# Kernel tuning notes

Hardware: AMD Instinct MI355X
Metric: run time of the kernel (lower is better)

Reference implementation:

```python
import jax, jax.numpy as jnp
import numpy as np

# ---- static configuration (mirrors init_kwargs) ----
B, NCAM = 1, 6
FC, FH, FW = 128, 16, 44              # featureShape
ORFH, ORFW = 128, 352                 # transformedImgShape H, W
D_ST, D_END, D_STEP = 1.0, 49.0, 1.0
D = int(np.arange(D_ST, D_END, D_STEP).shape[0])   # 48 depth bins
OUTC = 128
XB = (-50.0, 50.0, 1.0)
YB = (-50.0, 50.0, 1.0)
BEV_H = int((YB[1] - YB[0]) / YB[2])  # 100
BEV_W = int((XB[1] - XB[0]) / XB[2])  # 100
THRESH = 0.05                         # opacity_filter
ERR_TOL = 1.0                         # error_tolerance
COV_DILATE = 0.3                      # 3DGS low-pass on 2D cov diagonal
ALPHA_MAX = 0.99
ALPHA_MIN = 1.0 / 255.0
BN_EPS = 1e-3


def _frustum():
    ds = jnp.arange(D_ST, D_END, D_STEP, dtype=jnp.float32)[:, None, None]
    xs = jnp.linspace(0.0, ORFW - 1.0, FW, dtype=jnp.float32)[None, None, :]
    ys = jnp.linspace(0.0, ORFH - 1.0, FH, dtype=jnp.float32)[None, :, None]
    shp = (D, FH, FW)
    return jnp.stack([jnp.broadcast_to(xs, shp), jnp.broadcast_to(ys, shp),
                      jnp.broadcast_to(ds, shp)], axis=-1)  # [D,FH,FW,3]


def _conv(x, w, b, pad):
    y = jax.lax.conv_general_dilated(x, w, (1, 1), [(pad, pad), (pad, pad)],
                                     dimension_numbers=('NCHW', 'OIHW', 'NCHW'))
    return y + b[None, :, None, None]


def _bn(x, g, beta, m, v):
    # eval-mode BatchNorm2d with running stats
    inv = g / jnp.sqrt(v + BN_EPS)
    return (x - m[None, :, None, None]) * inv[None, :, None, None] + beta[None, :, None, None]


def _rasterize(features, means, cov6, opac):
    """Differentiable BEV Gaussian splatting (alpha compositing in index order).
    features [G,C], means [G,3] (normalized to [-1,1]), cov6 [G,6]=(xx,xy,xz,yy,yz,zz), opac [G].
    """
    h, w = BEV_H, BEV_W
    sh, sw = h / 2.0, w / 2.0                 # h/FoVy, w/FoVx with FoV=2
    op = jnp.where(opac > THRESH, opac, 0.0)  # opacity cull (variable-length mask in torch)
    # full_proj_transform: row0 -> row index (y), row1 -> col index (x)
    py = h / 2.0 - sh * means[:, 1]
    px = w / 2.0 - sw * means[:, 0]
    # 2D covariance in (py,px) basis: J Sigma3 J^T with J = [[0,-sh,0],[-sw,0,0]]
    a = sh * sh * cov6[:, 3] + COV_DILATE     # var along py (from Sigma_yy)
    b = sh * sw * cov6[:, 1]                  # cov(py,px) (from Sigma_xy)
    c = sw * sw * cov6[:, 0] + COV_DILATE     # var along px (from Sigma_xx)
    det = a * c - b * b
    op = jnp.where(det > 0.0, op, 0.0)
    inv_det = 1.0 / jnp.where(det > 0.0, det, 1.0)
    ys = jnp.arange(h, dtype=jnp.float32)
    xs = jnp.arange(w, dtype=jnp.float32)
    dy = py[None, :] - ys[:, None]            # [h,G]
    dx = px[None, :] - xs[:, None]            # [w,G]
    # power = -0.5 d^T Sigma2^{-1} d, Sigma2^{-1} = [[c,-b],[-b,a]]/det
    power = (-0.5 * (c * inv_det) * dy * dy)[:, None, :] \
            + (-0.5 * (a * inv_det) * dx * dx)[None, :, :] \
            + (b * inv_det) * dy[:, None, :] * dx[None, :, :]   # [h,w,G]
    alpha = jnp.minimum(ALPHA_MAX, op * jnp.exp(jnp.minimum(power, 0.0)))
    alpha = jnp.where(alpha < ALPHA_MIN, 0.0, alpha)
    T = jnp.cumprod(1.0 - alpha, axis=-1)
    T_excl = jnp.concatenate([jnp.ones_like(T[..., :1]), T[..., :-1]], axis=-1)
    wgt = alpha * T_excl                      # [h,w,G]
    bev = jnp.einsum('hwg,gc->chw', wgt, features)   # bg color = 0
    return bev


def reference(cam2ego_rot, cam2ego_trans, cam_intrins, post_cam2ego_rot, post_cam2ego_trans,
              img_feats, conv1_w, conv1_b, bn1_g, bn1_b, bn1_m, bn1_v,
              conv2_w, conv2_b, bn2_g, bn2_b, bn2_m, bn2_v, conv3_w, conv3_b):
    # --- geometry lifting ---
    frustum = _frustum()                                             # [D,FH,FW,3]
    pts = frustum[None, None] - post_cam2ego_trans[:, :, None, None, None, :]
    pts = jnp.einsum('bnij,bndhwj->bndhwi', jnp.linalg.inv(post_cam2ego_rot), pts)
    pts = jnp.concatenate([pts[..., :2] * pts[..., 2:3], pts[..., 2:3]], axis=-1)
    combine = cam2ego_rot @ jnp.linalg.inv(cam_intrins)
    geometry = jnp.einsum('bnij,bndhwj->bndhwi', combine, pts) \
               + cam2ego_trans[:, :, None, None, None, :]            # [B,N,D,FH,FW,3]
    # --- depth net ---
    x = img_feats.reshape(B * NCAM, FC, FH, FW)
    x = jax.nn.relu(_bn(_conv(x, conv1_w, conv1_b, 1), bn1_g, bn1_b, bn1_m, bn1_v))
    x = jax.nn.relu(_bn(_conv(x, conv2_w, conv2_b, 1), bn2_g, bn2_b, bn2_m, bn2_v))
    x = _conv(x, conv3_w, conv3_b, 0)                                # [B*N, OUTC+D+1, H, W]
    depth_prob = jax.nn.softmax(x[:, :D], axis=1).reshape(B, NCAM, D, FH, FW)
    opac = jax.nn.sigmoid(x[:, D:D + 1]).reshape(B, NCAM, FH, FW)
    feats = x[:, D + 1:].reshape(B, NCAM, OUTC, FH, FW)
    # --- per-pixel Gaussian moments over the depth distribution ---
    means3d = jnp.einsum('bndhw,bndhwi->bnhwi', depth_prob, geometry)
    delta = means3d[:, :, None] - geometry                           # [B,N,D,FH,FW,3]
    cov = jnp.einsum('bndhw,bndhwi,bndhwj->bnhwij', depth_prob, delta, delta)
    cov = cov * (ERR_TOL ** 2 / 9.0)
    # --- normalize to BEV frame ---
    center = jnp.array([(XB[0] + XB[1]) / 2.0, (YB[0] + YB[1]) / 2.0, 0.0], jnp.float32)
    scale = jnp.array([2.0 / (XB[1] - XB[0]), 2.0 / (YB[1] - YB[0]), 1.0], jnp.float32)
    means_n = (means3d - center) * scale
    cov_n = cov * (scale[:, None] * scale[None, :])
    cov6 = jnp.stack([cov_n[..., 0, 0], cov_n[..., 0, 1], cov_n[..., 0, 2],
                      cov_n[..., 1, 1], cov_n[..., 1, 2], cov_n[..., 2, 2]], axis=-1)
    G = NCAM * FH * FW
    f = jnp.transpose(feats, (0, 1, 3, 4, 2)).reshape(B, G, OUTC)
    m = means_n.reshape(B, G, 3)
    c6 = cov6.reshape(B, G, 6)
    o = opac.reshape(B, G)
    bev = jax.vmap(_rasterize)(f, m, c6, o)                          # [B,OUTC,BEV_H,BEV_W]
    return bev


def setup_inputs() -> dict:
    key = jax.random.key(0)
    ks = jax.random.split(key, 16)
    eye = jnp.eye(3, dtype=jnp.float32)
    cam2ego_rot = eye + 0.05 * jax.random.normal(ks[0], (B, NCAM, 3, 3), jnp.float32)
    cam2ego_trans = 0.5 * jax.random.normal(ks[1], (B, NCAM, 3), jnp.float32)
    intr = jnp.array([[260.0, 0.0, ORFW / 2.0], [0.0, 260.0, ORFH / 2.0], [0.0, 0.0, 1.0]], jnp.float32)
    cam_intrins = jnp.broadcast_to(intr, (B, NCAM, 3, 3)) * (1.0 + 0.01 * jax.random.normal(ks[2], (B, NCAM, 1, 1), jnp.float32))
    post_cam2ego_rot = eye + 0.01 * jax.random.normal(ks[3], (B, NCAM, 3, 3), jnp.float32)
    post_cam2ego_trans = 2.0 * jax.random.normal(ks[4], (B, NCAM, 3), jnp.float32)
    img_feats = jax.random.normal(ks[5], (B, NCAM, FC, FH, FW), jnp.float32)
    def cw(k, o, i, kh, kw):
        return jax.random.normal(k, (o, i, kh, kw), jnp.float32) / np.sqrt(i * kh * kw)
    inp = dict(cam2ego_rot=cam2ego_rot, cam2ego_trans=cam2ego_trans, cam_intrins=cam_intrins,
               post_cam2ego_rot=post_cam2ego_rot, post_cam2ego_trans=post_cam2ego_trans,
               img_feats=img_feats,
               conv1_w=cw(ks[6], FC, FC, 3, 3), conv1_b=jnp.zeros((FC,), jnp.float32),
               bn1_g=jnp.ones((FC,), jnp.float32), bn1_b=0.1 * jax.random.normal(ks[7], (FC,), jnp.float32),
               bn1_m=jnp.zeros((FC,), jnp.float32), bn1_v=jnp.ones((FC,), jnp.float32),
               conv2_w=cw(ks[8], FC, FC, 3, 3), conv2_b=jnp.zeros((FC,), jnp.float32),
               bn2_g=jnp.ones((FC,), jnp.float32), bn2_b=0.1 * jax.random.normal(ks[9], (FC,), jnp.float32),
               bn2_m=jnp.zeros((FC,), jnp.float32), bn2_v=jnp.ones((FC,), jnp.float32),
               conv3_w=cw(ks[10], OUTC + D + 1, FC, 1, 1),
               conv3_b=jnp.zeros((OUTC + D + 1,), jnp.float32))
    return inp
```

## Files before the change

kernel.cpp:

```cpp
#include <hip/hip_runtime.h>
#include <math.h>

#define NCAM 6
#define FHh 16
#define FWw 44
#define PIX 704
#define FCc 128
#define DB 48
#define C3 177
#define C3PAD 192
#define KCONV 1152
#define NG 4224
#define BEVN 10000
#define NSPLIT 3
#define SG 1408
#define TH_LOG (-5.5412635f)

#define OFF_WT1    0
#define OFF_WT2    147456
#define OFF_WT3    294912
#define OFF_GEO    319488
#define OFF_X1     724992
#define OFF_X2     1265664
#define OFF_X3     1806336
#define OFF_PART   2553984
#define OFF_PRM    4716672
#define OFF_PRM2   4733568
#define OFF_FEATT  4742016
#define OFF_SF     0
#define OFF_SP     3840000

typedef __attribute__((ext_vector_type(8))) short bf16x8;
typedef __attribute__((ext_vector_type(4))) float f32x4;
typedef __attribute__((ext_vector_type(4))) int i32x4;

__device__ __forceinline__ unsigned short f2bf(float x) {
  unsigned u = __float_as_uint(x);
  return (unsigned short)((u + 0x7FFF + ((u >> 16) & 1)) >> 16);
}
__device__ __forceinline__ float bf2f(unsigned short h) {
  return __uint_as_float(((unsigned)h) << 16);
}

__device__ __forceinline__ void inv3(const float* A, float* I) {
  float a=A[0],b=A[1],c=A[2],d=A[3],e=A[4],f=A[5],g=A[6],h=A[7],i=A[8];
  float c0 = e*i - f*h, c1 = f*g - d*i, c2 = d*h - e*g;
  float det = a*c0 + b*c1 + c*c2;
  float id = 1.f/det;
  I[0]=c0*id; I[1]=(c*h-b*i)*id; I[2]=(b*f-c*e)*id;
  I[3]=c1*id; I[4]=(a*i-c*g)*id; I[5]=(c*d-a*f)*id;
  I[6]=c2*id; I[7]=(b*g-a*h)*id; I[8]=(a*e-b*d)*id;
}

__global__ void k_geom(const float* __restrict__ rot, const float* __restrict__ intr,
                       const float* __restrict__ post_rot,
                       const float* __restrict__ trans, const float* __restrict__ post_trans,
                       float* __restrict__ ws) {
  __shared__ float sm[NCAM][24];
  if (threadIdx.x < NCAM) {
    int n = threadIdx.x;
    float ip[9], ii[9];
    inv3(post_rot + n*9, ip);
    inv3(intr + n*9, ii);
    const float* R = rot + n*9;
    for (int j = 0; j < 9; ++j) sm[n][j] = ip[j];
    for (int r = 0; r < 3; ++r)
      for (int c = 0; c < 3; ++c) {
        float s = 0.f;
        for (int k = 0; k < 3; ++k) s += R[r*3+k]*ii[k*3+c];
        sm[n][9 + r*3 + c] = s;
      }
  }
  __syncthreads();
  int idx = blockIdx.x*256 + threadIdx.x;
  if (idx >= NCAM*DB*PIX) return;
  int n = idx / (DB*PIX);
  int rem = idx % (DB*PIX);
  int d = rem / PIX;
  int hw = rem % PIX;
  int h = hw / FWw, w = hw % FWw;
  float fx = w * (351.0f/43.0f);
  float fy = h * (127.0f/15.0f);
  float fz = 1.0f + (float)d;
  const float* pt = post_trans + n*3;
  float v0 = fx - pt[0], v1 = fy - pt[1], v2 = fz - pt[2];
  const float* m = sm[n];
  float x = m[0]*v0 + m[1]*v1 + m[2]*v2;
  float y = m[3]*v0 + m[4]*v1 + m[5]*v2;
  float z = m[6]*v0 + m[7]*v1 + m[8]*v2;
  float q0 = x*z, q1 = y*z, q2 = z;
  const float* c = m + 9;
  const float* t = trans + n*3;
  float gx = c[0]*q0 + c[1]*q1 + c[2]*q2 + t[0];
  float gy = c[3]*q0 + c[4]*q1 + c[5]*q2 + t[1];
  ((float2*)(ws + OFF_GEO))[idx] = make_float2(gx, gy);
}

__global__ void k_wtrans(const float* __restrict__ w1, const float* __restrict__ w2,
                         const float* __restrict__ w3, float* __restrict__ ws) {
  int e = blockIdx.x*256 + threadIdx.x;
  if (e < 147456) {
    float v1 = w1[e], v2 = w2[e];
    unsigned short h1 = f2bf(v1), h2 = f2bf(v2);
    unsigned short l1 = f2bf(v1 - bf2f(h1)), l2 = f2bf(v2 - bf2f(h2));
    unsigned short* wt1 = (unsigned short*)(ws + OFF_WT1);
    unsigned short* wt2 = (unsigned short*)(ws + OFF_WT2);
    wt1[e] = h1; wt1[147456 + e] = l1;
    wt2[e] = h2; wt2[147456 + e] = l2;
  }
  if (e < 192*128) {
    int oc = e >> 7, k = e & 127;
    float v = (oc < C3) ? w3[oc*FCc + k] : 0.f;
    unsigned short h = f2bf(v);
    unsigned short* wt3 = (unsigned short*)(ws + OFF_WT3);
    wt3[e] = h; wt3[24576 + e] = f2bf(v - bf2f(h));
  }
}

#define LROW 20

__global__ __launch_bounds__(256) void k_gemm_mfma(
    const float* __restrict__ in, const float* ws, float* __restrict__ part, int woff)
{
  __shared__ int alds[2][64*LROW];
  __shared__ int blds[2][64*LROW];
  int tid = threadIdx.x;
  int px0 = blockIdx.x * 64;
  int oc0 = blockIdx.y * 64;
  int z = blockIdx.z; int n = z >> 2, ks = z & 3;
  const unsigned short* whi = (const unsigned short*)(ws + woff);
  const unsigned short* wlo = whi + 147456;
  const float* inn = in + (size_t)n*FCc*PIX;
  int wv = tid >> 6, lane = tid & 63;
  int a_oc = tid >> 2, a_kq = tid & 3;
  int b_px = tid & 63, b_kq = tid >> 6;
  int p = px0 + b_px; int b_y = p / FWw, b_x = p - b_y*FWw;
  int k00 = ks * 288;

  i32x4 pa_h, pa_l; float bv[8];
  auto issueA = [&](int s) {
    size_t gi = (size_t)(oc0 + a_oc)*KCONV + (k00 + s*32 + a_kq*8);
    pa_h = *(const i32x4*)(whi + gi);
    pa_l = *(const i32x4*)(wlo + gi);
  };
  auto issueB = [&](int s) {
    #pragma unroll
    for (int j = 0; j < 8; ++j) {
      int k = k00 + s*32 + b_kq*8 + j;
      int ic = k / 9, tap = k - ic*9;
      int ky = tap / 3, kx = tap - ky*3;
      int yy = b_y + ky - 1, xx = b_x + kx - 1;
      float v = 0.f;
      if ((unsigned)yy < FHh && (unsigned)xx < FWw) v = inn[(size_t)ic*PIX + yy*FWw + xx];
      bv[j] = v;
    }
  };

  f32x4 a00 = {0.f,0.f,0.f,0.f}, a01 = a00, a10 = a00, a11 = a00;
  int ocr = (wv >> 1) * 32, pxr = (wv & 1) * 32;
  int dq = (lane >> 4) * 4;
  int rA0 = (ocr + (lane & 15)) * LROW + dq;
  int rA1 = rA0 + 16*LROW;
  int rB0 = (pxr + (lane & 15)) * LROW + dq;
  int rB1 = rB0 + 16*LROW;
  int aw = a_oc*LROW + a_kq*4;
  int bw = b_px*LROW + b_kq*4;

  issueA(0); issueB(0);
  for (int s = 0; s < 9; ++s) {
    __syncthreads();
    *(i32x4*)&alds[0][aw] = pa_h;
    *(i32x4*)&alds[1][aw] = pa_l;
    {
      i32x4 vh, vl;
      int th[8], tl[8];
      #pragma unroll
      for (int j = 0; j < 8; ++j) {
        unsigned short h = f2bf(bv[j]);
        th[j] = h; tl[j] = f2bf(bv[j] - bf2f(h));
      }
      vh.x = th[0]|(th[1]<<16); vh.y = th[2]|(th[3]<<16);
      vh.z = th[4]|(th[5]<<16); vh.w = th[6]|(th[7]<<16);
      vl.x = tl[0]|(tl[1]<<16); vl.y = tl[2]|(tl[3]<<16);
      vl.z = tl[4]|(tl[5]<<16); vl.w = tl[6]|(tl[7]<<16);
      *(i32x4*)&blds[0][bw] = vh;
      *(i32x4*)&blds[1][bw] = vl;
    }
    __syncthreads();
    if (s < 8) { issueA(s+1); issueB(s+1); }
    bf16x8 ah0 = *(bf16x8*)&alds[0][rA0], ah1 = *(bf16x8*)&alds[0][rA1];
    bf16x8 al0 = *(bf16x8*)&alds[1][rA0], al1 = *(bf16x8*)&alds[1][rA1];
    bf16x8 bh0 = *(bf16x8*)&blds[0][rB0], bh1 = *(bf16x8*)&blds[0][rB1];
    bf16x8 bl0 = *(bf16x8*)&blds[1][rB0], bl1 = *(bf16x8*)&blds[1][rB1];
    a00 = __builtin_amdgcn_mfma_f32_16x16x32_bf16(ah0, bh0, a00, 0, 0, 0);
    a01 = __builtin_amdgcn_mfma_f32_16x16x32_bf16(ah0, bh1, a01, 0, 0, 0);
    a10 = __builtin_amdgcn_mfma_f32_16x16x32_bf16(ah1, bh0, a10, 0, 0, 0);
    a11 = __builtin_amdgcn_mfma_f32_16x16x32_bf16(ah1, bh1, a11, 0, 0, 0);
    a00 = __builtin_amdgcn_mfma_f32_16x16x32_bf16(ah0, bl0, a00, 0, 0, 0);
    a01 = __builtin_amdgcn_mfma_f32_16x16x32_bf16(ah0, bl1, a01, 0, 0, 0);
    a10 = __builtin_amdgcn_mfma_f32_16x16x32_bf16(ah1, bl0, a10, 0, 0, 0);
    a11 = __builtin_amdgcn_mfma_f32_16x16x32_bf16(ah1, bl1, a11, 0, 0, 0);
    a00 = __builtin_amdgcn_mfma_f32_16x16x32_bf16(al0, bh0, a00, 0, 0, 0);
    a01 = __builtin_amdgcn_mfma_f32_16x16x32_bf16(al0, bh1, a01, 0, 0, 0);
    a10 = __builtin_amdgcn_mfma_f32_16x16x32_bf16(al1, bh0, a10, 0, 0, 0);
    a11 = __builtin_amdgcn_mfma_f32_16x16x32_bf16(al1, bh1, a11, 0, 0, 0);
  }
  float* pp = part + (size_t)(ks*NCAM + n)*FCc*PIX;
  int ocb = oc0 + ocr + ((lane >> 4) << 2);
  int pxb = px0 + pxr + (lane & 15);
  #pragma unroll
  for (int i = 0; i < 4; ++i) {
    pp[(size_t)(ocb + i)*PIX + pxb]           = a00[i];
    pp[(size_t)(ocb + i)*PIX + pxb + 16]      = a01[i];
    pp[(size_t)(ocb + 16 + i)*PIX + pxb]      = a10[i];
    pp[(size_t)(ocb + 16 + i)*PIX + pxb + 16] = a11[i];
  }
}

__global__ __launch_bounds__(256) void k_gemm_mfma3(
    const float* __restrict__ in, const float* ws,
    const float* __restrict__ bias, float* __restrict__ outbuf)
{
  __shared__ int alds[2][64*LROW];
  __shared__ int blds[2][64*LROW];
  int tid = threadIdx.x;
  int px0 = blockIdx.x * 64;
  int oc0 = blockIdx.y * 64;
  int n = blockIdx.z;
  const unsigned short* whi = (const unsigned short*)(ws + OFF_WT3);
  const unsigned short* wlo = whi + 24576;
  const float* inn = in + (size_t)n*FCc*PIX;
  int wv = tid >> 6, lane = tid & 63;
  int a_oc = tid >> 2, a_kq = tid & 3;
  int b_px = tid & 63, b_kq = tid >> 6;
  int p = px0 + b_px;

  i32x4 pa_h, pa_l; float bvv[8];
  auto issueA = [&](int s) {
    size_t gi = (size_t)(oc0 + a_oc)*128 + (s*32 + a_kq*8);
    pa_h = *(const i32x4*)(whi + gi);
    pa_l = *(const i32x4*)(wlo + gi);
  };
  auto issueB = [&](int s) {
    #pragma unroll
    for (int j = 0; j < 8; ++j) {
      int ic = s*32 + b_kq*8 + j;
      bvv[j] = inn[(size_t)ic*PIX + p];
    }
  };

  f32x4 a00 = {0.f,0.f,0.f,0.f}, a01 = a00, a10 = a00, a11 = a00;
  int ocr = (wv >> 1) * 32, pxr = (wv & 1) * 32;
  int dq = (lane >> 4) * 4;
  int rA0 = (ocr + (lane & 15)) * LROW + dq;
  int rA1 = rA0 + 16*LROW;
  int rB0 = (pxr + (lane & 15)) * LROW + dq;
  int rB1 = rB0 + 16*LROW;
  int aw = a_oc*LROW + a_kq*4;
  int bw = b_px*LROW + b_kq*4;

  issueA(0); issueB(0);
  for (int s = 0; s < 4; ++s) {
    __syncthreads();
    *(i32x4*)&alds[0][aw] = pa_h;
    *(i32x4*)&alds[1][aw] = pa_l;
    {
      i32x4 vh, vl;
      int th[8], tl[8];
      #pragma unroll
      for (int j = 0; j < 8; ++j) {
        unsigned short h = f2bf(bvv[j]);
        th[j] = h; tl[j] = f2bf(bvv[j] - bf2f(h));
      }
      vh.x = th[0]|(th[1]<<16); vh.y = th[2]|(th[3]<<16);
      vh.z = th[4]|(th[5]<<16); vh.w = th[6]|(th[7]<<16);
      vl.x = tl[0]|(tl[1]<<16); vl.y = tl[2]|(tl[3]<<16);
      vl.z = tl[4]|(tl[5]<<16); vl.w = tl[6]|(tl[7]<<16);
      *(i32x4*)&blds[0][bw] = vh;
      *(i32x4*)&blds[1][bw] = vl;
    }
    __syncthreads();
    if (s < 3) { issueA(s+1); issueB(s+1); }
    bf16x8 ah0 = *(bf16x8*)&alds[0][rA0], ah1 = *(bf16x8*)&alds[0][rA1];
    bf16x8 al0 = *(bf16x8*)&alds[1][rA0], al1 = *(bf16x8*)&alds[1][rA1];
    bf16x8 bh0 = *(bf16x8*)&blds[0][rB0], bh1 = *(bf16x8*)&blds[0][rB1];
    bf16x8 bl0 = *(bf16x8*)&blds[1][rB0], bl1 = *(bf16x8*)&blds[1][rB1];
    a00 = __builtin_amdgcn_mfma_f32_16x16x32_bf16(ah0, bh0, a00, 0, 0, 0);
    a01 = __builtin_amdgcn_mfma_f32_16x16x32_bf16(ah0, bh1, a01, 0, 0, 0);
    a10 = __builtin_amdgcn_mfma_f32_16x16x32_bf16(ah1, bh0, a10, 0, 0, 0);
    a11 = __builtin_amdgcn_mfma_f32_16x16x32_bf16(ah1, bh1, a11, 0, 0, 0);
    a00 = __builtin_amdgcn_mfma_f32_16x16x32_bf16(ah0, bl0, a00, 0, 0, 0);
    a01 = __builtin_amdgcn_mfma_f32_16x16x32_bf16(ah0, bl1, a01, 0, 0, 0);
    a10 = __builtin_amdgcn_mfma_f32_16x16x32_bf16(ah1, bl0, a10, 0, 0, 0);
    a11 = __builtin_amdgcn_mfma_f32_16x16x32_bf16(ah1, bl1, a11, 0, 0, 0);
    a00 = __builtin_amdgcn_mfma_f32_16x16x32_bf16(al0, bh0, a00, 0, 0, 0);
    a01 = __builtin_amdgcn_mfma_f32_16x16x32_bf16(al0, bh1, a01, 0, 0, 0);
    a10 = __builtin_amdgcn_mfma_f32_16x16x32_bf16(al1, bh0, a10, 0, 0, 0);
    a11 = __builtin_amdgcn_mfma_f32_16x16x32_bf16(al1, bh1, a11, 0, 0, 0);
  }
  int ocb = oc0 + ocr + ((lane >> 4) << 2);
  int pxb = px0 + pxr + (lane & 15);
  #pragma unroll
  for (int i = 0; i < 4; ++i) {
    int o0 = ocb + i, o1 = ocb + 16 + i;
    if (o0 < C3) {
      float b = bias[o0];
      outbuf[(size_t)(n*C3 + o0)*PIX + pxb]      = a00[i] + b;
      outbuf[(size_t)(n*C3 + o0)*PIX + pxb + 16] = a01[i] + b;
    }
    if (o1 < C3) {
      float b = bias[o1];
      outbuf[(size_t)(n*C3 + o1)*PIX + pxb]      = a10[i] + b;
      outbuf[(size_t)(n*C3 + o1)*PIX + pxb + 16] = a11[i] + b;
    }
  }
}

__global__ void k_epi_bn(const float* __restrict__ part, const float* __restrict__ cb,
                         const float* __restrict__ g, const float* __restrict__ be,
                         const float* __restrict__ mn, const float* __restrict__ vr,
                         float* __restrict__ out, int KSPLIT)
{
  int idx = blockIdx.x*256 + threadIdx.x;
  if (idx >= NCAM*FCc*176) return;
  int px4 = idx % 176;
  int t = idx / 176;
  int oc = t % FCc;
  int n = t / FCc;
  float4 s = {0.f,0.f,0.f,0.f};
  for (int ks = 0; ks < KSPLIT; ++ks) {
    const float4* p = (const float4*)(part + (size_t)((ks*NCAM+n)*FCc + oc)*PIX);
    float4 v = p[px4];
    s.x += v.x; s.y += v.y; s.z += v.z; s.w += v.w;
  }
  float inv = g[oc] * rsqrtf(vr[oc] + 1e-3f);
  float sh = (cb[oc] - mn[oc]) * inv + be[oc];
  float4 o;
  o.x = fmaxf(s.x*inv + sh, 0.f);
  o.y = fmaxf(s.y*inv + sh, 0.f);
  o.z = fmaxf(s.z*inv + sh, 0.f);
  o.w = fmaxf(s.w*inv + sh, 0.f);
  ((float4*)(out + (size_t)(n*FCc + oc)*PIX))[px4] = o;
}

__global__ void k_moments(float* __restrict__ ws) {
  int wid  = (blockIdx.x * 256 + threadIdx.x) >> 6;
  int lane = threadIdx.x & 63;
  int n = wid / PIX, hw = wid % PIX;
  const float* x3 = ws + OFF_X3 + (size_t)n*C3*PIX + hw;
  float logit = (lane < DB) ? x3[(size_t)lane*PIX] : -1e30f;
  float mx = logit;
  for (int off = 1; off < 64; off <<= 1) mx = fmaxf(mx, __shfl_xor(mx, off));
  float e = (lane < DB) ? expf(logit - mx) : 0.f;
  float s = e;
  for (int off = 1; off < 64; off <<= 1) s += __shfl_xor(s, off);
  float p = e / s;
  float gx = 0.f, gy = 0.f;
  if (lane < DB) {
    float2 g2 = ((const float2*)(ws + OFF_GEO))[(size_t)(n*DB + lane)*PIX + hw];
    gx = g2.x; gy = g2.y;
  }
  float sx = p*gx;
  for (int off = 1; off < 64; off <<= 1) sx += __shfl_xor(sx, off);
  float sy = p*gy;
  for (int off = 1; off < 64; off <<= 1) sy += __shfl_xor(sy, off);
  float dx = gx - sx, dy = gy - sy;
  float c00 = p*dx*dx, c01 = p*dx*dy, c11 = p*dy*dy;
  for (int off = 1; off < 64; off <<= 1) c00 += __shfl_xor(c00, off);
  for (int off = 1; off < 64; off <<= 1) c01 += __shfl_xor(c01, off);
  for (int off = 1; off < 64; off <<= 1) c11 += __shfl_xor(c11, off);
  float opl = x3[(size_t)DB*PIX];
  float opac = 1.f / (1.f + expf(-opl));
  float a = c11*(1.f/9.f) + 0.3f;
  float b = c01*(1.f/9.f);
  float c = c00*(1.f/9.f) + 0.3f;
  float py = 50.f - sy;
  float px = 50.f - sx;
  float det = a*c - b*b;
  float op = (opac > 0.05f) ? opac : 0.f;
  float invd = 1.f;
  if (det > 0.f) invd = 1.f/det; else op = 0.f;
  if (lane == 0) {
    float lop = (op > 0.f) ? logf(op) : -1e30f;
    ((float4*)(ws + OFF_PRM))[wid]  = make_float4(py, px, -0.5f*c*invd, -0.5f*a*invd);
    ((float2*)(ws + OFF_PRM2))[wid] = make_float2(b*invd, lop);
  }
  float* ft = ws + OFF_FEATT + (size_t)wid*128;
  ft[lane]      = x3[(size_t)(DB + 1 + lane)*PIX];
  ft[lane + 64] = x3[(size_t)(DB + 1 + lane + 64)*PIX];
}

template<int CTRL, int RMASK>
__device__ __forceinline__ float dpp_mul(float v) {
  int t = __builtin_amdgcn_update_dpp(0x3f800000, __float_as_int(v), CTRL, RMASK, 0xF, false);
  return v * __int_as_float(t);
}

__global__ __launch_bounds__(512) void k_raster(const float* __restrict__ ws,
                                                float* __restrict__ wsout) {
  __shared__ float4 s4[SG];
  __shared__ float2 s2[SG];
  int lane = threadIdx.x & 63, wv = threadIdx.x >> 6;
  int split = blockIdx.x / 1250;
  int pxb   = blockIdx.x % 1250;
  int pix = pxb * 8 + wv;
  float yi = (float)(pix / 100), xi = (float)(pix % 100);
  int gbase = split * SG;
  const float4* prm4 = (const float4*)(ws + OFF_PRM) + gbase;
  const float2* prm2 = (const float2*)(ws + OFF_PRM2) + gbase;
  const float2* ft = (const float2*)(ws + OFF_FEATT);
  for (int i = threadIdx.x; i < SG; i += 512) {
    s4[i] = prm4[i];
    s2[i] = prm2[i];
  }
  __syncthreads();
  float T = 1.f, ax = 0.f, ay = 0.f;
  for (int gl = 0; gl < SG; gl += 64) {
    float4 c4 = s4[gl + lane];
    float2 c2 = s2[gl + lane];
    float dyv = c4.x - yi, dxv = c4.y - xi;
    float pw = c4.z*dyv*dyv + c4.w*dxv*dxv + c2.x*dyv*dxv;
    float t  = pw + c2.y;
    bool hit = (t >= TH_LOG);
    unsigned long long m0 = __ballot(hit);
    if (m0) {
      float alpha = __expf(fminf(t, c2.y));
      alpha = fminf(alpha, 0.99f);
      alpha = hit ? alpha : 0.f;
      float P = 1.f - alpha;
      P = dpp_mul<0x111, 0xF>(P);
      P = dpp_mul<0x112, 0xF>(P);
      P = dpp_mul<0x114, 0xF>(P);
      P = dpp_mul<0x118, 0xF>(P);
      P = dpp_mul<0x142, 0xA>(P);
      P = dpp_mul<0x143, 0xC>(P);
      float E = __int_as_float(__builtin_amdgcn_update_dpp(
                  0x3f800000, __float_as_int(P), 0x138, 0xF, 0xF, false));
      float w = alpha * T * E;
      T *= __int_as_float(__builtin_amdgcn_readlane(__float_as_int(P), 63));
      unsigned long long mask = __ballot(w > 1e-9f);
      int g0 = gbase + gl;
      while (mask) {
        int jj[8];
        #pragma unroll
        for (int b = 0; b < 8; ++b) {
          if (mask) { jj[b] = __builtin_ctzll(mask); mask &= mask - 1ull; }
          else jj[b] = -1;
        }
        float2 fb[8]; float wb[8];
        #pragma unroll
        for (int b = 0; b < 8; ++b) {
          int j = (jj[b] >= 0) ? jj[b] : jj[0];
          fb[b] = ft[(size_t)(g0 + j)*64 + lane];
          wb[b] = (jj[b] >= 0)
            ? __int_as_float(__builtin_amdgcn_readlane(__float_as_int(w), jj[b]))
            : 0.f;
        }
        #pragma unroll
        for (int b = 0; b < 8; ++b) { ax += wb[b]*fb[b].x; ay += wb[b]*fb[b].y; }
      }
      if (T < 1e-7f) break;
    }
  }
  float* sf = wsout + OFF_SF + ((size_t)split*BEVN + pix)*128;
  sf[2*lane]   = ax;
  sf[2*lane+1] = ay;
  if (lane == 0) (wsout + OFF_SP)[split*BEVN + pix] = T;
}

__global__ __launch_bounds__(512) void k_combine(const float* __restrict__ ws,
                                                 float* __restrict__ out) {
  int lane = threadIdx.x & 63, wv = threadIdx.x >> 6;
  int pix = blockIdx.x * 8 + wv;
  const float* sp = ws + OFF_SP;
  float P0 = sp[pix], P1 = sp[BEVN + pix];
  const float2* f0 = (const float2*)(ws + OFF_SF + (size_t)pix*128);
  const float2* f1 = (const float2*)(ws + OFF_SF + ((size_t)BEVN + pix)*128);
  const float2* f2 = (const float2*)(ws + OFF_SF + ((size_t)2*BEVN + pix)*128);
  float2 a = f0[lane], b = f1[lane], c = f2[lane];
  float w1 = P0, w2 = P0*P1;
  float ox = a.x + w1*b.x + w2*c.x;
  float oy = a.y + w1*b.y + w2*c.y;
  out[(size_t)(2*lane)*BEVN + pix]   = ox;
  out[(size_t)(2*lane+1)*BEVN + pix] = oy;
}

extern "C" void kernel_launch(void* const* d_in, const int* in_sizes, int n_in,
                              void* d_out, int out_size, void* d_ws, size_t ws_size,
                              hipStream_t stream) {
  const float* rot        = (const float*)d_in[0];
  const float* trans      = (const float*)d_in[1];
  const float* intr       = (const float*)d_in[2];
  const float* post_rot   = (const float*)d_in[3];
  const float* post_trans = (const float*)d_in[4];
  const float* img        = (const float*)d_in[5];
  const float* w1  = (const float*)d_in[6];
  const float* b1  = (const float*)d_in[7];
  const float* g1  = (const float*)d_in[8];
  const float* be1 = (const float*)d_in[9];
  const float* m1  = (const float*)d_in[10];
  const float* v1  = (const float*)d_in[11];
  const float* w2  = (const float*)d_in[12];
  const float* b2  = (const float*)d_in[13];
  const float* g2  = (const float*)d_in[14];
  const float* be2 = (const float*)d_in[15];
  const float* m2  = (const float*)d_in[16];
  const float* v2  = (const float*)d_in[17];
  const float* w3  = (const float*)d_in[18];
  const float* b3  = (const float*)d_in[19];
  float* ws  = (float*)d_ws;
  float* out = (float*)d_out;

  k_wtrans<<<576, 256, 0, stream>>>(w1, w2, w3, ws);
  k_geom<<<792, 256, 0, stream>>>(rot, intr, post_rot, trans, post_trans, ws);

  k_gemm_mfma<<<dim3(11,2,24), 256, 0, stream>>>(img, ws, ws+OFF_PART, OFF_WT1);
  k_epi_bn<<<528, 256, 0, stream>>>(ws+OFF_PART, b1, g1, be1, m1, v1, ws+OFF_X1, 4);
  k_gemm_mfma<<<dim3(11,2,24), 256, 0, stream>>>(ws+OFF_X1, ws, ws+OFF_PART, OFF_WT2);
  k_epi_bn<<<528, 256, 0, stream>>>(ws+OFF_PART, b2, g2, be2, m2, v2, ws+OFF_X2, 4);
  k_gemm_mfma3<<<dim3(11,3,6), 256, 0, stream>>>(ws+OFF_X2, ws, b3, ws+OFF_X3);

  k_moments<<<1056, 256, 0, stream>>>(ws);
  k_raster<<<3750, 512, 0, stream>>>(ws, ws);
  k_combine<<<1250, 512, 0, stream>>>(ws, out);
}
```

Before: 123.4 us.

## Drop split-K conv GEMM, fuse BN-ReLU epilogue, merge prep kernels

The two 3x3 conv GEMMs no longer split K four ways into partial buffers followed by a separate BN+ReLU reduction kernel. Each block now computes a 32x32 output tile over the full K=1152 in 36 steps and applies bias, BatchNorm and ReLU directly in its epilogue. The weight-transform and geometry kernels are merged into one launch. This removes two kernel launches per conv plus the partial-sum round trip through memory. In exchange each block runs a much longer serial K loop with one small MFMA tile per wave, which gives less reuse per LDS load.

```diff
diff --git a/kernel.cpp b/kernel.cpp
--- a/kernel.cpp
+++ b/kernel.cpp
@@ -8,7 +8,6 @@
 #define FCc 128
 #define DB 48
 #define C3 177
-#define C3PAD 192
 #define KCONV 1152
 #define NG 4224
 #define BEVN 10000
@@ -23,7 +22,6 @@
 #define OFF_X1     724992
 #define OFF_X2     1265664
 #define OFF_X3     1806336
-#define OFF_PART   2553984
 #define OFF_PRM    4716672
 #define OFF_PRM2   4733568
 #define OFF_FEATT  4742016
@@ -33,6 +31,7 @@
 typedef __attribute__((ext_vector_type(8))) short bf16x8;
 typedef __attribute__((ext_vector_type(4))) float f32x4;
 typedef __attribute__((ext_vector_type(4))) int i32x4;
+typedef __attribute__((ext_vector_type(2))) int i32x2;
 
 __device__ __forceinline__ unsigned short f2bf(float x) {
   unsigned u = __float_as_uint(x);
@@ -52,101 +51,103 @@
   I[6]=c2*id; I[7]=(b*g-a*h)*id; I[8]=(a*e-b*d)*id;
 }
 
-__global__ void k_geom(const float* __restrict__ rot, const float* __restrict__ intr,
+__global__ void k_prep(const float* __restrict__ rot, const float* __restrict__ intr,
                        const float* __restrict__ post_rot,
                        const float* __restrict__ trans, const float* __restrict__ post_trans,
-                       float* __restrict__ ws) {
-  __shared__ float sm[NCAM][24];
-  if (threadIdx.x < NCAM) {
-    int n = threadIdx.x;
-    float ip[9], ii[9];
-    inv3(post_rot + n*9, ip);
-    inv3(intr + n*9, ii);
-    const float* R = rot + n*9;
-    for (int j = 0; j < 9; ++j) sm[n][j] = ip[j];
-    for (int r = 0; r < 3; ++r)
-      for (int c = 0; c < 3; ++c) {
-        float s = 0.f;
-        for (int k = 0; k < 3; ++k) s += R[r*3+k]*ii[k*3+c];
-        sm[n][9 + r*3 + c] = s;
-      }
-  }
-  __syncthreads();
-  int idx = blockIdx.x*256 + threadIdx.x;
-  if (idx >= NCAM*DB*PIX) return;
-  int n = idx / (DB*PIX);
-  int rem = idx % (DB*PIX);
-  int d = rem / PIX;
-  int hw = rem % PIX;
-  int h = hw / FWw, w = hw % FWw;
-  float fx = w * (351.0f/43.0f);
-  float fy = h * (127.0f/15.0f);
-  float fz = 1.0f + (float)d;
-  const float* pt = post_trans + n*3;
-  float v0 = fx - pt[0], v1 = fy - pt[1], v2 = fz - pt[2];
-  const float* m = sm[n];
-  float x = m[0]*v0 + m[1]*v1 + m[2]*v2;
-  float y = m[3]*v0 + m[4]*v1 + m[5]*v2;
-  float z = m[6]*v0 + m[7]*v1 + m[8]*v2;
-  float q0 = x*z, q1 = y*z, q2 = z;
-  const float* c = m + 9;
-  const float* t = trans + n*3;
-  float gx = c[0]*q0 + c[1]*q1 + c[2]*q2 + t[0];
-  float gy = c[3]*q0 + c[4]*q1 + c[5]*q2 + t[1];
-  ((float2*)(ws + OFF_GEO))[idx] = make_float2(gx, gy);
-}
-
-__global__ void k_wtrans(const float* __restrict__ w1, const float* __restrict__ w2,
-                         const float* __restrict__ w3, float* __restrict__ ws) {
-  int e = blockIdx.x*256 + threadIdx.x;
-  if (e < 147456) {
-    float v1 = w1[e], v2 = w2[e];
-    unsigned short h1 = f2bf(v1), h2 = f2bf(v2);
-    unsigned short l1 = f2bf(v1 - bf2f(h1)), l2 = f2bf(v2 - bf2f(h2));
-    unsigned short* wt1 = (unsigned short*)(ws + OFF_WT1);
-    unsigned short* wt2 = (unsigned short*)(ws + OFF_WT2);
-    wt1[e] = h1; wt1[147456 + e] = l1;
-    wt2[e] = h2; wt2[147456 + e] = l2;
-  }
-  if (e < 192*128) {
-    int oc = e >> 7, k = e & 127;
-    float v = (oc < C3) ? w3[oc*FCc + k] : 0.f;
-    unsigned short h = f2bf(v);
-    unsigned short* wt3 = (unsigned short*)(ws + OFF_WT3);
-    wt3[e] = h; wt3[24576 + e] = f2bf(v - bf2f(h));
+                       const float* __restrict__ w1, const float* __restrict__ w2,
+                       const float* __restrict__ w3, float* __restrict__ ws) {
+  if (blockIdx.x < 792) {
+    __shared__ float sm[NCAM][24];
+    if (threadIdx.x < NCAM) {
+      int n = threadIdx.x;
+      float ip[9], ii[9];
+      inv3(post_rot + n*9, ip);
+      inv3(intr + n*9, ii);
+      const float* R = rot + n*9;
+      for (int j = 0; j < 9; ++j) sm[n][j] = ip[j];
+      for (int r = 0; r < 3; ++r)
+        for (int c = 0; c < 3; ++c) {
+          float s = 0.f;
+          for (int k = 0; k < 3; ++k) s += R[r*3+k]*ii[k*3+c];
+          sm[n][9 + r*3 + c] = s;
+        }
+    }
+    __syncthreads();
+    int idx = blockIdx.x*256 + threadIdx.x;
+    if (idx >= NCAM*DB*PIX) return;
+    int n = idx / (DB*PIX);
+    int rem = idx % (DB*PIX);
+    int d = rem / PIX;
+    int hw = rem % PIX;
+    int h = hw / FWw, w = hw % FWw;
+    float fx = w * (351.0f/43.0f);
+    float fy = h * (127.0f/15.0f);
+    float fz = 1.0f + (float)d;
+    const float* pt = post_trans + n*3;
+    float v0 = fx - pt[0], v1 = fy - pt[1], v2 = fz - pt[2];
+    const float* m = sm[n];
+    float x = m[0]*v0 + m[1]*v1 + m[2]*v2;
+    float y = m[3]*v0 + m[4]*v1 + m[5]*v2;
+    float z = m[6]*v0 + m[7]*v1 + m[8]*v2;
+    float q0 = x*z, q1 = y*z, q2 = z;
+    const float* c = m + 9;
+    const float* t = trans + n*3;
+    float gx = c[0]*q0 + c[1]*q1 + c[2]*q2 + t[0];
+    float gy = c[3]*q0 + c[4]*q1 + c[5]*q2 + t[1];
+    ((float2*)(ws + OFF_GEO))[idx] = make_float2(gx, gy);
+  } else {
+    int e = (blockIdx.x - 792)*256 + threadIdx.x;
+    if (e < 147456) {
+      float v1 = w1[e], v2 = w2[e];
+      unsigned short h1 = f2bf(v1), h2 = f2bf(v2);
+      unsigned short l1 = f2bf(v1 - bf2f(h1)), l2 = f2bf(v2 - bf2f(h2));
+      unsigned short* wt1 = (unsigned short*)(ws + OFF_WT1);
+      unsigned short* wt2 = (unsigned short*)(ws + OFF_WT2);
+      wt1[e] = h1; wt1[147456 + e] = l1;
+      wt2[e] = h2; wt2[147456 + e] = l2;
+    }
+    if (e < 192*128) {
+      int oc = e >> 7, k = e & 127;
+      float v = (oc < C3) ? w3[oc*FCc + k] : 0.f;
+      unsigned short h = f2bf(v);
+      unsigned short* wt3 = (unsigned short*)(ws + OFF_WT3);
+      wt3[e] = h; wt3[24576 + e] = f2bf(v - bf2f(h));
+    }
   }
 }
 
 #define LROW 20
 
-__global__ __launch_bounds__(256) void k_gemm_mfma(
-    const float* __restrict__ in, const float* ws, float* __restrict__ part, int woff)
+__global__ __launch_bounds__(256) void k_gemm_mfma32(
+    const float* __restrict__ in, const float* ws, int woff,
+    const float* __restrict__ cb, const float* __restrict__ g,
+    const float* __restrict__ be, const float* __restrict__ mn,
+    const float* __restrict__ vr, float* __restrict__ outbuf)
 {
-  __shared__ int alds[2][64*LROW];
-  __shared__ int blds[2][64*LROW];
+  __shared__ int alds[2][32*LROW];
+  __shared__ int blds[2][32*LROW];
   int tid = threadIdx.x;
-  int px0 = blockIdx.x * 64;
-  int oc0 = blockIdx.y * 64;
-  int z = blockIdx.z; int n = z >> 2, ks = z & 3;
+  int px0 = blockIdx.x * 32;
+  int oc0 = blockIdx.y * 32;
+  int n = blockIdx.z;
   const unsigned short* whi = (const unsigned short*)(ws + woff);
   const unsigned short* wlo = whi + 147456;
   const float* inn = in + (size_t)n*FCc*PIX;
   int wv = tid >> 6, lane = tid & 63;
-  int a_oc = tid >> 2, a_kq = tid & 3;
-  int b_px = tid & 63, b_kq = tid >> 6;
+  int a_oc = tid >> 3, a_kq = tid & 7;
+  int b_px = tid & 31, b_kq = tid >> 5;
   int p = px0 + b_px; int b_y = p / FWw, b_x = p - b_y*FWw;
-  int k00 = ks * 288;
-
-  i32x4 pa_h, pa_l; float bv[8];
+
+  i32x2 pa_h, pa_l; float bv[4];
   auto issueA = [&](int s) {
-    size_t gi = (size_t)(oc0 + a_oc)*KCONV + (k00 + s*32 + a_kq*8);
-    pa_h = *(const i32x4*)(whi + gi);
-    pa_l = *(const i32x4*)(wlo + gi);
+    size_t gi = (size_t)(oc0 + a_oc)*KCONV + (s*32 + a_kq*4);
+    pa_h = *(const i32x2*)(whi + gi);
+    pa_l = *(const i32x2*)(wlo + gi);
   };
   auto issueB = [&](int s) {
     #pragma unroll
-    for (int j = 0; j < 8; ++j) {
-      int k = k00 + s*32 + b_kq*8 + j;
+    for (int j = 0; j < 4; ++j) {
+      int k = s*32 + b_kq*4 + j;
       int ic = k / 9, tap = k - ic*9;
       int ky = tap / 3, kx = tap - ky*3;
       int yy = b_y + ky - 1, xx = b_x + kx - 1;
@@ -156,64 +157,50 @@
     }
   };
 
-  f32x4 a00 = {0.f,0.f,0.f,0.f}, a01 = a00, a10 = a00, a11 = a00;
-  int ocr = (wv >> 1) * 32, pxr = (wv & 1) * 32;
+  f32x4 acc = {0.f,0.f,0.f,0.f};
+  int ocr = (wv >> 1) * 16, pxr = (wv & 1) * 16;
   int dq = (lane >> 4) * 4;
-  int rA0 = (ocr + (lane & 15)) * LROW + dq;
-  int rA1 = rA0 + 16*LROW;
-  int rB0 = (pxr + (lane & 15)) * LROW + dq;
-  int rB1 = rB0 + 16*LROW;
-  int aw = a_oc*LROW + a_kq*4;
-  int bw = b_px*LROW + b_kq*4;
+  int rA = (ocr + (lane & 15)) * LROW + dq;
+  int rB = (pxr + (lane & 15)) * LROW + dq;
+  int aw = a_oc*LROW + a_kq*2;
+  int bw = b_px*LROW + b_kq*2;
 
   issueA(0); issueB(0);
-  for (int s = 0; s < 9; ++s) {
+  for (int s = 0; s < 36; ++s) {
     __syncthreads();
-    *(i32x4*)&alds[0][aw] = pa_h;
-    *(i32x4*)&alds[1][aw] = pa_l;
+    *(i32x2*)&alds[0][aw] = pa_h;
+    *(i32x2*)&alds[1][aw] = pa_l;
     {
-      i32x4 vh, vl;
-      int th[8], tl[8];
+      i32x2 vh, vl;
+      int th[4], tl[4];
       #pragma unroll
-      for (int j = 0; j < 8; ++j) {
+      for (int j = 0; j < 4; ++j) {
         unsigned short h = f2bf(bv[j]);
         th[j] = h; tl[j] = f2bf(bv[j] - bf2f(h));
       }
       vh.x = th[0]|(th[1]<<16); vh.y = th[2]|(th[3]<<16);
-      vh.z = th[4]|(th[5]<<16); vh.w = th[6]|(th[7]<<16);
       vl.x = tl[0]|(tl[1]<<16); vl.y = tl[2]|(tl[3]<<16);
-      vl.z = tl[4]|(tl[5]<<16); vl.w = tl[6]|(tl[7]<<16);
-      *(i32x4*)&blds[0][bw] = vh;
-      *(i32x4*)&blds[1][bw] = vl;
+      *(i32x2*)&blds[0][bw] = vh;
+      *(i32x2*)&blds[1][bw] = vl;
     }
     __syncthreads();
-    if (s < 8) { issueA(s+1); issueB(s+1); }
-    bf16x8 ah0 = *(bf16x8*)&alds[0][rA0], ah1 = *(bf16x8*)&alds[0][rA1];
-    bf16x8 al0 = *(bf16x8*)&alds[1][rA0], al1 = *(bf16x8*)&alds[1][rA1];
-    bf16x8 bh0 = *(bf16x8*)&blds[0][rB0], bh1 = *(bf16x8*)&blds[0][rB1];
-    bf16x8 bl0 = *(bf16x8*)&blds[1][rB0], bl1 = *(bf16x8*)&blds[1][rB1];
-    a00 = __builtin_amdgcn_mfma_f32_16x16x32_bf16(ah0, bh0, a00, 0, 0, 0);
-    a01 = __builtin_amdgcn_mfma_f32_16x16x32_bf16(ah0, bh1, a01, 0, 0, 0);
-    a10 = __builtin_amdgcn_mfma_f32_16x16x32_bf16(ah1, bh0, a10, 0, 0, 0);
-    a11 = __builtin_amdgcn_mfma_f32_16x16x32_bf16(ah1, bh1, a11, 0, 0, 0);
-    a00 = __builtin_amdgcn_mfma_f32_16x16x32_bf16(ah0, bl0, a00, 0, 0, 0);
-    a01 = __builtin_amdgcn_mfma_f32_16x16x32_bf16(ah0, bl1, a01, 0, 0, 0);
-    a10 = __builtin_amdgcn_mfma_f32_16x16x32_bf16(ah1, bl0, a10, 0, 0, 0);
-    a11 = __builtin_amdgcn_mfma_f32_16x16x32_bf16(ah1, bl1, a11, 0, 0, 0);
-    a00 = __builtin_amdgcn_mfma_f32_16x16x32_bf16(al0, bh0, a00, 0, 0, 0);
-    a01 = __builtin_amdgcn_mfma_f32_16x16x32_bf16(al0, bh1, a01, 0, 0, 0);
-    a10 = __builtin_amdgcn_mfma_f32_16x16x32_bf16(al1, bh0, a10, 0, 0, 0);
-    a11 = __builtin_amdgcn_mfma_f32_16x16x32_bf16(al1, bh1, a11, 0, 0, 0);
-  }
-  float* pp = part + (size_t)(ks*NCAM + n)*FCc*PIX;
+    if (s < 35) { issueA(s+1); issueB(s+1); }
+    bf16x8 ah = *(bf16x8*)&alds[0][rA];
+    bf16x8 al = *(bf16x8*)&alds[1][rA];
+    bf16x8 bh = *(bf16x8*)&blds[0][rB];
+    bf16x8 bl = *(bf16x8*)&blds[1][rB];
+    acc = __builtin_amdgcn_mfma_f32_16x16x32_bf16(ah, bh, acc, 0, 0, 0);
+    acc = __builtin_amdgcn_mfma_f32_16x16x32_bf16(ah, bl, acc, 0, 0, 0);
+    acc = __builtin_amdgcn_mfma_f32_16x16x32_bf16(al, bh, acc, 0, 0, 0);
+  }
   int ocb = oc0 + ocr + ((lane >> 4) << 2);
   int pxb = px0 + pxr + (lane & 15);
   #pragma unroll
   for (int i = 0; i < 4; ++i) {
-    pp[(size_t)(ocb + i)*PIX + pxb]           = a00[i];
-    pp[(size_t)(ocb + i)*PIX + pxb + 16]      = a01[i];
-    pp[(size_t)(ocb + 16 + i)*PIX + pxb]      = a10[i];
-    pp[(size_t)(ocb + 16 + i)*PIX + pxb + 16] = a11[i];
+    int oc = ocb + i;
+    float inv = g[oc] * rsqrtf(vr[oc] + 1e-3f);
+    float sh = (cb[oc] - mn[oc]) * inv + be[oc];
+    outbuf[(size_t)(n*FCc + oc)*PIX + pxb] = fmaxf(acc[i]*inv + sh, 0.f);
   }
 }
 
@@ -314,33 +301,6 @@
       outbuf[(size_t)(n*C3 + o1)*PIX + pxb + 16] = a11[i] + b;
     }
   }
-}
-
-__global__ void k_epi_bn(const float* __restrict__ part, const float* __restrict__ cb,
-                         const float* __restrict__ g, const float* __restrict__ be,
-                         const float* __restrict__ mn, const float* __restrict__ vr,
-                         float* __restrict__ out, int KSPLIT)
-{
-  int idx = blockIdx.x*256 + threadIdx.x;
-  if (idx >= NCAM*FCc*176) return;
-  int px4 = idx % 176;
-  int t = idx / 176;
-  int oc = t % FCc;
-  int n = t / FCc;
-  float4 s = {0.f,0.f,0.f,0.f};
-  for (int ks = 0; ks < KSPLIT; ++ks) {
-    const float4* p = (const float4*)(part + (size_t)((ks*NCAM+n)*FCc + oc)*PIX);
-    float4 v = p[px4];
-    s.x += v.x; s.y += v.y; s.z += v.z; s.w += v.w;
-  }
-  float inv = g[oc] * rsqrtf(vr[oc] + 1e-3f);
-  float sh = (cb[oc] - mn[oc]) * inv + be[oc];
-  float4 o;
-  o.x = fmaxf(s.x*inv + sh, 0.f);
-  o.y = fmaxf(s.y*inv + sh, 0.f);
-  o.z = fmaxf(s.z*inv + sh, 0.f);
-  o.w = fmaxf(s.w*inv + sh, 0.f);
-  ((float4*)(out + (size_t)(n*FCc + oc)*PIX))[px4] = o;
 }
 
 __global__ void k_moments(float* __restrict__ ws) {
@@ -511,13 +471,13 @@
   float* ws  = (float*)d_ws;
   float* out = (float*)d_out;
 
-  k_wtrans<<<576, 256, 0, stream>>>(w1, w2, w3, ws);
-  k_geom<<<792, 256, 0, stream>>>(rot, intr, post_rot, trans, post_trans, ws);
-
-  k_gemm_mfma<<<dim3(11,2,24), 256, 0, stream>>>(img, ws, ws+OFF_PART, OFF_WT1);
-  k_epi_bn<<<528, 256, 0, stream>>>(ws+OFF_PART, b1, g1, be1, m1, v1, ws+OFF_X1, 4);
-  k_gemm_mfma<<<dim3(11,2,24), 256, 0, stream>>>(ws+OFF_X1, ws, ws+OFF_PART, OFF_WT2);
-  k_epi_bn<<<528, 256, 0, stream>>>(ws+OFF_PART, b2, g2, be2, m2, v2, ws+OFF_X2, 4);
+  k_prep<<<1368, 256, 0, stream>>>(rot, intr, post_rot, trans, post_trans,
+                                   w1, w2, w3, ws);
+
+  k_gemm_mfma32<<<dim3(22,4,6), 256, 0, stream>>>(img, ws, OFF_WT1,
+                                                  b1, g1, be1, m1, v1, ws+OFF_X1);
+  k_gemm_mfma32<<<dim3(22,4,6), 256, 0, stream>>>(ws+OFF_X1, ws, OFF_WT2,
+                                                  b2, g2, be2, m2, v2, ws+OFF_X2);
   k_gemm_mfma3<<<dim3(11,3,6), 256, 0, stream>>>(ws+OFF_X2, ws, b3, ws+OFF_X3);
 
   k_moments<<<1056, 256, 0, stream>>>(ws);
```

Result: slower. 142.2 us (+15.3%).
